# Kernel tuning notes

Measured on AMD Instinct MI355X. Metric: run time of the kernel, lower is better.

Reference implementation:

```python
import jax, jax.numpy as jnp
import numpy as np

N_ATOMS = 10000
N_EDGES = 200000
L_MAX = 2
K_L = [32, 24, 16]  # k_max_l = n_element_channels * n_max_l

# (l1, l2, L) in the original loop order (l1 outer, l2 inner, L ascending)
PAIRS = [(0,0,0),(0,1,1),(0,2,2),
         (1,0,1),(1,1,0),(1,1,1),(1,1,2),(1,2,1),(1,2,2),
         (2,0,2),(2,1,1),(2,1,2),(2,2,0),(2,2,1),(2,2,2)]
# concatenated input width -> k_max_l[L] per (L, sigma) channel
LIN = {'0_1': (72, 32), '1_1': (80, 24), '1_m1': (40, 24), '2_1': (72, 16), '2_m1': (32, 16)}


def setup_inputs() -> dict:
    key = jax.random.key(0)
    it = iter(jax.random.split(key, 64))
    def nrm(shape):
        return jax.random.normal(next(it), shape, dtype=jnp.float32)
    inp = {}
    for l in range(L_MAX + 1):
        inp['rb%d' % l] = nrm((N_EDGES, K_L[l]))           # radial basis per l
    for l in range(L_MAX + 1):
        inp['sh%d' % l] = nrm((N_EDGES, 2*l+1, 1))         # spherical harmonics per l
    inp['emb'] = nrm((N_ATOMS, 1, K_L[0]))                 # initial center embedding
    for l in range(L_MAX + 1):
        inp['f%d' % l] = nrm((N_ATOMS, 2*l+1, K_L[l]))     # nu=1 equivariant features
    for (l1, l2, L) in PAIRS:
        inp['cg_%d_%d_%d' % (l1, l2, L)] = nrm(((2*l1+1)*(2*l2+1), 2*L+1))
    for LS, (fin, fout) in LIN.items():
        inp['W_' + LS] = nrm((fin, fout)) / np.float32(np.sqrt(fin))
        inp['b_' + LS] = nrm((fout,)) * 0.01
    inp['centers'] = jax.random.randint(next(it), (N_EDGES,), 0, N_ATOMS)
    inp['neighbors'] = jax.random.randint(next(it), (N_EDGES,), 0, N_ATOMS)
    inp['n_atoms'] = N_ATOMS
    return inp


def _normalize(x, dims):
    # Normalizer(dims): RMS normalization over the given dims
    return x * jax.lax.rsqrt(jnp.mean(x * x, axis=dims, keepdims=True) + 1e-12)


def _forward(floats, centers, neighbors, n_atoms):
    (rb0, rb1, rb2, sh0, sh1, sh2, emb, f0, f1, f2,
     cg_0_0_0, cg_0_1_1, cg_0_2_2, cg_1_0_1, cg_1_1_0, cg_1_1_1, cg_1_1_2,
     cg_1_2_1, cg_1_2_2, cg_2_0_2, cg_2_1_1, cg_2_1_2, cg_2_2_0, cg_2_2_1,
     cg_2_2_2, W_0_1, b_0_1, W_1_1, b_1_1, W_1_m1, b_1_m1, W_2_1, b_2_1,
     W_2_m1, b_2_m1) = floats
    rb = [rb0, rb1, rb2]; sh = [sh0, sh1, sh2]; feats = [f0, f1, f2]
    cgs = {'0_0_0': cg_0_0_0, '0_1_1': cg_0_1_1, '0_2_2': cg_0_2_2,
           '1_0_1': cg_1_0_1, '1_1_0': cg_1_1_0, '1_1_1': cg_1_1_1,
           '1_1_2': cg_1_1_2, '1_2_1': cg_1_2_1, '1_2_2': cg_1_2_2,
           '2_0_2': cg_2_0_2, '2_1_1': cg_2_1_1, '2_1_2': cg_2_1_2,
           '2_2_0': cg_2_2_0, '2_2_1': cg_2_2_1, '2_2_2': cg_2_2_2}
    lin = {'0_1': (W_0_1, b_0_1), '1_1': (W_1_1, b_1_1), '1_m1': (W_1_m1, b_1_m1),
           '2_1': (W_2_1, b_2_1), '2_m1': (W_2_m1, b_2_m1)}

    # ---- InvariantMessagePasser: density_l = scatter_add over centers of
    #      sh_l * rb_l * emb[neighbors]
    emb_n = emb[neighbors]                                       # [E, 1, k0]
    densities = []
    for l in range(L_MAX + 1):
        msg = sh[l] * rb[l][:, None, :] * emb_n[:, :, :K_L[l]]   # [E, 2l+1, k_l]
        densities.append(jax.ops.segment_sum(msg, centers, num_segments=n_atoms))

    # ---- EquivariantMessagePasser
    ve = [sh[l] * rb[l][:, None, :] for l in range(L_MAX + 1)]   # vector expansion [E,2l+1,k_l]
    fn = [feats[l][neighbors] for l in range(L_MAX + 1)]         # gathered neighbor feats
    results = {}
    for (l1, l2, L) in PAIRS:
        S = (-1) ** (l1 + l2 + L)
        k = min(K_L[l1], K_L[l2])
        t1 = ve[l1][:, :, :k]                                    # [E, 2l1+1, k]
        t2 = fn[l2][:, :, :k]                                    # [E, 2l2+1, k]
        cg = cgs['%d_%d_%d' % (l1, l2, L)].reshape(2*l1+1, 2*l2+1, 2*L+1)
        # fused outer product + CG contraction -> [E, 2L+1, k]
        res = jnp.einsum('eak,ebk,abM->eMk', t1, t2, cg)
        pooled = jax.ops.segment_sum(res, centers, num_segments=n_atoms)
        LS = '%d_%s' % (L, 'm1' if S < 0 else '1')
        results.setdefault(LS, []).append(pooled)

    outs = {}
    for LS, (W, b) in lin.items():
        x = jnp.concatenate(results[LS], axis=2)                 # [n_atoms, 2L+1, size_LS]
        x = _normalize(x, (0, 1))
        x = jnp.einsum('amf,fk->amk', x, W) + b
        outs[LS] = _normalize(x, (0, 1, 2))

    return (densities[0], densities[1], densities[2],
            outs['0_1'], outs['1_1'], outs['1_m1'], outs['2_1'], outs['2_m1'])


def reference(rb0, rb1, rb2, sh0, sh1, sh2, emb, f0, f1, f2,
              cg_0_0_0, cg_0_1_1, cg_0_2_2, cg_1_0_1, cg_1_1_0, cg_1_1_1,
              cg_1_1_2, cg_1_2_1, cg_1_2_2, cg_2_0_2, cg_2_1_1, cg_2_1_2,
              cg_2_2_0, cg_2_2_1, cg_2_2_2, W_0_1, b_0_1, W_1_1, b_1_1,
              W_1_m1, b_1_m1, W_2_1, b_2_1, W_2_m1, b_2_m1,
              centers, neighbors, n_atoms):
    floats = (rb0, rb1, rb2, sh0, sh1, sh2, emb, f0, f1, f2,
              cg_0_0_0, cg_0_1_1, cg_0_2_2, cg_1_0_1, cg_1_1_0, cg_1_1_1,
              cg_1_1_2, cg_1_2_1, cg_1_2_2, cg_2_0_2, cg_2_1_1, cg_2_1_2,
              cg_2_2_0, cg_2_2_1, cg_2_2_2, W_0_1, b_0_1, W_1_1, b_1_1,
              W_1_m1, b_1_m1, W_2_1, b_2_1, W_2_m1, b_2_m1)
    return _forward(floats, centers, neighbors, n_atoms)
```

## Files before the change

kernel.cpp:

```cpp
#include <hip/hip_runtime.h>
#include <hip/hip_bf16.h>

typedef __hip_bfloat16 bf16;

#define N_ATOMS 10000
#define N_EDGES 200000

#define SCG   0
#define SINV  616
#define SS1P  1024
#define SS2P  19968
#define SWS2  20288
#define SINTS 20352
#define IFLAG  0
#define ICOUNT 16
#define IOFFS  10016
#define ICURS  20032
#define IELIST 30032
#define INTS_END 430032
#define SXACC (SINTS + INTS_END)
#define BIG_FLOATS (SXACC + 952*N_ATOMS)

#define O0 0
#define O1 320000
// ... 20 lines not shown
__constant__ int c_fin[5]   = {72,80,40,72,32};
__constant__ int c_kout[5]  = {32,24,24,16,16};
__constant__ int c_yoff[5]  = {OY+0, OY+320000, OY+1040000, OY+1760000, OY+2560000};
__constant__ int c_numel[5] = {320000,720000,720000,800000,800000};
__constant__ int c_cum[6]   = {0,32,104,176,256,336};
__constant__ int c_xb[5]    = {0,72,312,432,792};
__constant__ int c_Ms[5]    = {1,3,3,5,5};

__global__ void k_zero(float* wsf, int* wsi,
                       const unsigned short* rb0u, const unsigned short* embu) {
  if (blockIdx.x == 0 && threadIdx.x < 64) {
    int lane = threadIdx.x;
    int bad = 0;
    for (int i = lane; i < 256; i += 64) {
      unsigned u1 = ((unsigned)rb0u[2*i]) << 16;
      unsigned u2 = ((unsigned)embu[2*i]) << 16;
      float v1 = __uint_as_float(u1);
      float v2 = __uint_as_float(u2);
      if (!(fabsf(v1) < 1e9f) || !(fabsf(v2) < 1e9f)) bad = 1;
    }
    unsigned long long any = __ballot(bad);
    if (lane == 0) wsi[IFLAG] = (any != 0ULL) ? 1 : 0;
  }
  int i = blockIdx.x*blockDim.x + threadIdx.x;
  if (i < N_ATOMS) wsi[ICOUNT + i] = 0;
  int j = i - N_ATOMS;
  if (j >= 0 && j < N_ATOMS) wsi[ICURS + j] = 0;
  j -= N_ATOMS;
  if (j >= 0 && j < 18944) wsf[SS1P + j] = 0.f;
  j -= 18944;
  if (j >= 0 && j < 325) wsf[SS2P + j] = 0.f;
}

template<typename T>
__global__ void k_cg(Ptrs15 cg, float* wsf, const int* flag) {
  if (flag[0] != dtid<T>()) return;
  int i = blockIdx.x*blockDim.x + threadIdx.x;
  if (i >= 615) return;
  int s = 0, off = i;
  while (off >= c_cg_sizes[s]) { off -= c_cg_sizes[s]; ++s; }
  wsf[SCG + i] = ldv((const T*)cg.p[s], off);
}

__global__ void k_hist(const int* __restrict__ centers, int* __restrict__ counts) {
  int e = blockIdx.x*blockDim.x + threadIdx.x;
  if (e < N_EDGES) atomicAdd(&counts[centers[e]], 1);
}

__global__ void k_scan(const int* __restrict__ counts, int* __restrict__ offs) {
  __shared__ int part[1024];
  int t = threadIdx.x;
  int base = t*10;
  int s = 0;
  for (int i = 0; i < 10; ++i) { int idx = base+i; if (idx < N_ATOMS) s += counts[idx]; }
  part[t] = s;
  __syncthreads();
  for (int d = 1; d < 1024; d <<= 1) {
    int v = part[t];
    int add = (t >= d) ? part[t-d] : 0;
    __syncthreads();
    part[t] = v + add;
    __syncthreads();
  }
  int run = (t == 0) ? 0 : part[t-1];
  for (int i = 0; i < 10; ++i) {
    int idx = base+i;
    if (idx < N_ATOMS) { offs[idx] = run; run += counts[idx]; }
  }
  if (t == 1023) offs[N_ATOMS] = part[1023];
}

__global__ void k_scatter2(const int* __restrict__ centers, const int* __restrict__ neighbors,
                           const int* __restrict__ offs, int* __restrict__ cursors,
                           int2* __restrict__ elist2) {
  int e = blockIdx.x*blockDim.x + threadIdx.x;
  if (e < N_EDGES) {
    int c = centers[e];
    int p = atomicAdd(&cursors[c], 1);
    elist2[offs[c] + p] = make_int2(e, neighbors[e]);
  }
}

template<typename T>
__global__ __launch_bounds__(128) void k_role(
    const T* __restrict__ rb0, const T* __restrict__ rb1, const T* __restrict__ rb2,
    const T* __restrict__ sh0, const T* __restrict__ sh1, const T* __restrict__ sh2,
    const T* __restrict__ emb, const T* __restrict__ f0, const T* __restrict__ f1,
    const T* __restrict__ f2, const int2* __restrict__ el2,
    const int* __restrict__ offs, const float* __restrict__ cgf,
    float* __restrict__ s1p, float* __restrict__ xout, T* __restrict__ out,
    const int* __restrict__ flag)
{
  if (flag[0] != dtid<T>()) return;
  int lane = threadIdx.x & 63;
  int g = blockIdx.x * 2 + (threadIdx.x >> 6);
  int a = g / 5;
  int role = g - a*5;
  int beg = offs[a];
  int cnt = offs[a+1] - beg;
  const int2* eb = el2 + beg;
  int ab = a & 63;
  int k32 = lane & 31, e2 = lane >> 5;
  int k16 = lane & 15, e4 = lane >> 4;
  float* xg = xout + a*952;
  float* s1r = s1p + ab*296;

  if (role == 0) {
    float acc[8];
    #pragma unroll
    for (int i = 0; i < 8; ++i) acc[i] = 0.f;
    for (int base = 0; base < cnt; base += 4) {
      #pragma unroll
      for (int u = 0; u < 2; ++u) {
        int idx = base + 2*u + e2;
        float w = (idx < cnt) ? 1.f : 0.f;
        int ic  = (idx < cnt) ? idx : 0;
        int2 en = eb[ic];
        int e = en.x, n = en.y;
        float s0 = ldv(sh0, e);
        float s1a0 = ldv(sh1, e*3+0), s1a1 = ldv(sh1, e*3+1), s1a2 = ldv(sh1, e*3+2);
        float rb0k = ldv(rb0, e*32 + k32) * w;
        float ek   = ldv(emb, n*32 + k32);
        float f0k  = ldv(f0,  n*32 + k32);
        float ve0 = s0 * rb0k;
        acc[0] = fmaf(ve0, ek, acc[0]);
        acc[4] = fmaf(ve0, f0k, acc[4]);
        if (k32 < 24) {
          float rb1k = ldv(rb1, e*24 + k32) * w;
          float rbek = rb1k * ek;
          acc[1] = fmaf(s1a0, rbek, acc[1]);
          acc[2] = fmaf(s1a1, rbek, acc[2]);
          acc[3] = fmaf(s1a2, rbek, acc[3]);
          float f1k0 = ldv(f1, n*72 + k32);
          float f1k1 = ldv(f1, n*72 + 24 + k32);
          float f1k2 = ldv(f1, n*72 + 48 + k32);
          acc[5] = fmaf(ve0, f1k0, acc[5]);
          acc[6] = fmaf(ve0, f1k1, acc[6]);
          acc[7] = fmaf(ve0, f1k2, acc[7]);
        }
      }
    }
    #pragma unroll
    for (int i = 0; i < 8; ++i) acc[i] += __shfl_xor(acc[i], 32);
    float x000 = cgf[0] * acc[4];
    const float* C011 = cgf + 1;
    float x011[3];
    #pragma unroll
    for (int M = 0; M < 3; ++M) {
      float t = 0.f;
      #pragma unroll
      for (int b = 0; b < 3; ++b) t = fmaf(acc[5+b], C011[b*3+M], t);
      x011[M] = t;
    }
    if (lane < 32) {
      stv(out, O0 + a*32 + k32, acc[0]);
      xg[k32] = x000;
      atomicAdd(&s1r[k32], x000*x000);
      if (k32 < 24) {
        #pragma unroll
        for (int m = 0; m < 3; ++m) stv(out, O1 + a*72 + m*24 + k32, acc[1+m]);
        #pragma unroll
        for (int M = 0; M < 3; ++M) xg[72+M*80+k32] = x011[M];
        atomicAdd(&s1r[72+k32], x011[0]*x011[0]+x011[1]*x011[1]+x011[2]*x011[2]);
      }
    }
  } else if (role == 1) {
    float acc[12];
    #pragma unroll
    for (int i = 0; i < 12; ++i) acc[i] = 0.f;
    int k24 = (k32 < 24) ? k32 : 23;
    float m24 = (k32 < 24) ? 1.f : 0.f;
    for (int base = 0; base < cnt; base += 4) {
      #pragma unroll
      for (int u = 0; u < 2; ++u) {
        int idx = base + 2*u + e2;
        float w = ((idx < cnt) ? 1.f : 0.f) * m24;
        int ic  = (idx < cnt) ? idx : 0;
        int2 en = eb[ic];
        int e = en.x, n = en.y;
        float s1a0 = ldv(sh1, e*3+0), s1a1 = ldv(sh1, e*3+1), s1a2 = ldv(sh1, e*3+2);
        float rb1k = ldv(rb1, e*24 + k24) * w;
        float f0k  = ldv(f0,  n*32 + k24);
        float f1k0 = ldv(f1, n*72 + k24);
        float f1k1 = ldv(f1, n*72 + 24 + k24);
        float f1k2 = ldv(f1, n*72 + 48 + k24);
        float g3 = rb1k * f0k;
        acc[0] = fmaf(g3, s1a0, acc[0]);
        acc[1] = fmaf(g3, s1a1, acc[1]);
        acc[2] = fmaf(g3, s1a2, acc[2]);
        float sa;
        sa = rb1k * s1a0;
        acc[3] = fmaf(sa, f1k0, acc[3]); acc[4] = fmaf(sa, f1k1, acc[4]); acc[5] = fmaf(sa, f1k2, acc[5]);
        sa = rb1k * s1a1;
        acc[6] = fmaf(sa, f1k0, acc[6]); acc[7] = fmaf(sa, f1k1, acc[7]); acc[8] = fmaf(sa, f1k2, acc[8]);
        sa = rb1k * s1a2;
        acc[9] = fmaf(sa, f1k0, acc[9]); acc[10] = fmaf(sa, f1k1, acc[10]); acc[11] = fmaf(sa, f1k2, acc[11]);
      }
    }
    #pragma unroll
    for (int i = 0; i < 12; ++i) acc[i] += __shfl_xor(acc[i], 32);
    const float* C101 = cgf + 35;
    const float* C110 = cgf + 44;
    const float* C111 = cgf + 53;
    const float* C112 = cgf + 80;
    float x101[3], x111[3], x112[5], x110;
    #pragma unroll
    for (int M = 0; M < 3; ++M) {
      float t = 0.f;
      #pragma unroll
      for (int aa = 0; aa < 3; ++aa) t = fmaf(acc[aa], C101[aa*3+M], t);
      x101[M] = t;
    }
    {
      float t = 0.f;
      #pragma unroll
      for (int q = 0; q < 9; ++q) t = fmaf(acc[3+q], C110[q], t);
      x110 = t;
    }
    #pragma unroll
    for (int M = 0; M < 3; ++M) {
      float t = 0.f;
      #pragma unroll
      for (int q = 0; q < 9; ++q) t = fmaf(acc[3+q], C111[q*3+M], t);
      x111[M] = t;
    }
    #pragma unroll
    for (int M = 0; M < 5; ++M) {
      float t = 0.f;
      #pragma unroll
      for (int q = 0; q < 9; ++q) t = fmaf(acc[3+q], C112[q*5+M], t);
      x112[M] = t;
    }
    if (lane < 24) {
      xg[32+k32] = x110;
      #pragma unroll
      for (int M = 0; M < 3; ++M) xg[72+M*80+24+k32] = x101[M];
      #pragma unroll
      for (int M = 0; M < 3; ++M) xg[312+M*40+k32]   = x111[M];
      #pragma unroll
      for (int M = 0; M < 5; ++M) xg[432+M*72+16+k32] = x112[M];
      atomicAdd(&s1r[32+k32], x110*x110);
      atomicAdd(&s1r[96+k32], x101[0]*x101[0]+x101[1]*x101[1]+x101[2]*x101[2]);
      atomicAdd(&s1r[152+k32], x111[0]*x111[0]+x111[1]*x111[1]+x111[2]*x111[2]);
      atomicAdd(&s1r[208+k32], x112[0]*x112[0]+x112[1]*x112[1]+x112[2]*x112[2]
                              + x112[3]*x112[3]+x112[4]*x112[4]);
    }
  } else if (role == 2) {
    float acc[25];
    #pragma unroll
    for (int i = 0; i < 25; ++i) acc[i] = 0.f;
    for (int base = 0; base < cnt; base += 8) {
      #pragma unroll
      for (int u = 0; u < 2; ++u) {
        int idx = base + 4*u + e4;
        float w = (idx < cnt) ? 1.f : 0.f;
        int ic  = (idx < cnt) ? idx : 0;
        int2 en = eb[ic];
        int e = en.x, n = en.y;
        float s0 = ldv(sh0, e);
        float s1a[3];
        #pragma unroll
        for (int m = 0; m < 3; ++m) s1a[m] = ldv(sh1, e*3+m);
        float s2a[5];
        #pragma unroll
        for (int m = 0; m < 5; ++m) s2a[m] = ldv(sh2, e*5+m);
        float rb0k = ldv(rb0, e*32 + k16) * w;
        float rb1k = ldv(rb1, e*24 + k16) * w;
        float rb2k = ldv(rb2, e*16 + k16) * w;
        float ek   = ldv(emb, n*32 + k16);
        float f2k[5];
        #pragma unroll
        for (int b = 0; b < 5; ++b) f2k[b] = ldv(f2, n*80 + b*16 + k16);
        float re = rb2k * ek;
        #pragma unroll
        for (int m = 0; m < 5; ++m) acc[m] = fmaf(s2a[m], re, acc[m]);
        float ve0 = s0 * rb0k;
        #pragma unroll
        for (int b = 0; b < 5; ++b) acc[5+b] = fmaf(ve0, f2k[b], acc[5+b]);
        #pragma unroll
        for (int aa = 0; aa < 3; ++aa) {
          float sa = rb1k * s1a[aa];
          #pragma unroll
          for (int b = 0; b < 5; ++b)
            acc[10+aa*5+b] = fmaf(sa, f2k[b], acc[10+aa*5+b]);
        }
      }
    }
    #pragma unroll
    for (int i = 0; i < 25; ++i) {
      acc[i] += __shfl_xor(acc[i], 16);
      acc[i] += __shfl_xor(acc[i], 32);
    }
    const float* C022 = cgf + 10;
    const float* C121 = cgf + 125;
    const float* C122 = cgf + 170;
    float x022[5], x121[3], x122[5];
    #pragma unroll
    for (int M = 0; M < 5; ++M) {
      float t = 0.f;
      #pragma unroll
      for (int b = 0; b < 5; ++b) t = fmaf(acc[5+b], C022[b*5+M], t);
      x022[M] = t;
    }
    #pragma unroll
    for (int M = 0; M < 3; ++M) {
      float t = 0.f;
      #pragma unroll
      for (int q = 0; q < 15; ++q) t = fmaf(acc[10+q], C121[q*3+M], t);
      x121[M] = t;
    }
    #pragma unroll
    for (int M = 0; M < 5; ++M) {
      float t = 0.f;
      #pragma unroll
      for (int q = 0; q < 15; ++q) t = fmaf(acc[10+q], C122[q*5+M], t);
      x122[M] = t;
    }
    if (lane < 16) {
      #pragma unroll
      for (int m = 0; m < 5; ++m) stv(out, O2 + a*80 + m*16 + k16, acc[m]);
      #pragma unroll
      for (int M = 0; M < 5; ++M) xg[432+M*72+k16]   = x022[M];
      #pragma unroll
      for (int M = 0; M < 3; ++M) xg[72+M*80+48+k16] = x121[M];
      #pragma unroll
      for (int M = 0; M < 5; ++M) xg[792+M*32+k16]   = x122[M];
      atomicAdd(&s1r[192+k16], x022[0]*x022[0]+x022[1]*x022[1]+x022[2]*x022[2]
                              + x022[3]*x022[3]+x022[4]*x022[4]);
      atomicAdd(&s1r[120+k16], x121[0]*x121[0]+x121[1]*x121[1]+x121[2]*x121[2]);
      atomicAdd(&s1r[264+k16], x122[0]*x122[0]+x122[1]*x122[1]+x122[2]*x122[2]
                              + x122[3]*x122[3]+x122[4]*x122[4]);
    }
  } else if (role == 3) {
    float acc[20];
    #pragma unroll
    for (int i = 0; i < 20; ++i) acc[i] = 0.f;
    for (int base = 0; base < cnt; base += 8) {
      #pragma unroll
      for (int u = 0; u < 2; ++u) {
        int idx = base + 4*u + e4;
        float w = (idx < cnt) ? 1.f : 0.f;
        int ic  = (idx < cnt) ? idx : 0;
        int2 en = eb[ic];
        int e = en.x, n = en.y;
        float s2a[5];
        #pragma unroll
        for (int m = 0; m < 5; ++m) s2a[m] = ldv(sh2, e*5+m);
        float rb2k = ldv(rb2, e*16 + k16) * w;
        float f0k  = ldv(f0,  n*32 + k16);
        float f1k[3];
        #pragma unroll
        for (int b = 0; b < 3; ++b) f1k[b] = ldv(f1, n*72 + b*24 + k16);
        float g9 = rb2k * f0k;
        #pragma unroll
        for (int aa = 0; aa < 5; ++aa) acc[aa] = fmaf(g9, s2a[aa], acc[aa]);
        #pragma unroll
        for (int aa = 0; aa < 5; ++aa) {
          float sa = rb2k * s2a[aa];
          #pragma unroll
          for (int b = 0; b < 3; ++b)
            acc[5+aa*3+b] = fmaf(sa, f1k[b], acc[5+aa*3+b]);
        }
      }
    }
    #pragma unroll
    for (int i = 0; i < 20; ++i) {
      acc[i] += __shfl_xor(acc[i], 16);
      acc[i] += __shfl_xor(acc[i], 32);
    }
    const float* C202 = cgf + 245;
    const float* C211 = cgf + 270;
    const float* C212 = cgf + 315;
    float x202[5], x211[3], x212[5];
    #pragma unroll
    for (int M = 0; M < 5; ++M) {
      float t = 0.f;
      #pragma unroll
      for (int aa = 0; aa < 5; ++aa) t = fmaf(acc[aa], C202[aa*5+M], t);
      x202[M] = t;
    }
    #pragma unroll
    for (int M = 0; M < 3; ++M) {
      float t = 0.f;
      #pragma unroll
      for (int q = 0; q < 15; ++q) t = fmaf(acc[5+q], C211[q*3+M], t);
      x211[M] = t;
    }
    #pragma unroll
    for (int M = 0; M < 5; ++M) {
      float t = 0.f;
      #pragma unroll
      for (int q = 0; q < 15; ++q) t = fmaf(acc[5+q], C212[q*5+M], t);
      x212[M] = t;
    }
    if (lane < 16) {
      #pragma unroll
      for (int M = 0; M < 5; ++M) xg[432+M*72+40+k16] = x202[M];
      #pragma unroll
      for (int M = 0; M < 3; ++M) xg[72+M*80+64+k16]  = x211[M];
      #pragma unroll
      for (int M = 0; M < 5; ++M) xg[792+M*32+16+k16] = x212[M];
      atomicAdd(&s1r[232+k16], x202[0]*x202[0]+x202[1]*x202[1]+x202[2]*x202[2]
                              + x202[3]*x202[3]+x202[4]*x202[4]);
      atomicAdd(&s1r[136+k16], x211[0]*x211[0]+x211[1]*x211[1]+x211[2]*x211[2]);
      atomicAdd(&s1r[280+k16], x212[0]*x212[0]+x212[1]*x212[1]+x212[2]*x212[2]
                              + x212[3]*x212[3]+x212[4]*x212[4]);
    }
  } else {
    float acc[25];
    #pragma unroll
    for (int i = 0; i < 25; ++i) acc[i] = 0.f;
    for (int base = 0; base < cnt; base += 8) {
      #pragma unroll
      for (int u = 0; u < 2; ++u) {
        int idx = base + 4*u + e4;
        float w = (idx < cnt) ? 1.f : 0.f;
        int ic  = (idx < cnt) ? idx : 0;
        int2 en = eb[ic];
        int e = en.x, n = en.y;
        float s2a[5];
        #pragma unroll
        for (int m = 0; m < 5; ++m) s2a[m] = ldv(sh2, e*5+m);
        float rb2k = ldv(rb2, e*16 + k16) * w;
        float f2k[5];
        #pragma unroll
        for (int b = 0; b < 5; ++b) f2k[b] = ldv(f2, n*80 + b*16 + k16);
        #pragma unroll
        for (int aa = 0; aa < 5; ++aa) {
          float sa = rb2k * s2a[aa];
          #pragma unroll
          for (int b = 0; b < 5; ++b)
            acc[aa*5+b] = fmaf(sa, f2k[b], acc[aa*5+b]);
        }
      }
    }
    #pragma unroll
    for (int i = 0; i < 25; ++i) {
      acc[i] += __shfl_xor(acc[i], 16);
      acc[i] += __shfl_xor(acc[i], 32);
    }
    const float* C220 = cgf + 390;
    const float* C221 = cgf + 415;
    const float* C222 = cgf + 490;
    float x220, x221[3], x222[5];
    {
      float t = 0.f;
      #pragma unroll
      for (int q = 0; q < 25; ++q) t = fmaf(acc[q], C220[q], t);
      x220 = t;
    }
    #pragma unroll
    for (int M = 0; M < 3; ++M) {
      float t = 0.f;
      #pragma unroll
      for (int q = 0; q < 25; ++q) t = fmaf(acc[q], C221[q*3+M], t);
      x221[M] = t;
    }
    #pragma unroll
    for (int M = 0; M < 5; ++M) {
      float t = 0.f;
      #pragma unroll
      for (int q = 0; q < 25; ++q) t = fmaf(acc[q], C222[q*5+M], t);
      x222[M] = t;
    }
    if (lane < 16) {
      xg[56+k16] = x220;
      #pragma unroll
      for (int M = 0; M < 3; ++M) xg[312+M*40+24+k16] = x221[M];
      #pragma unroll
      for (int M = 0; M < 5; ++M) xg[432+M*72+56+k16] = x222[M];
      atomicAdd(&s1r[56+k16], x220*x220);
      atomicAdd(&s1r[176+k16], x221[0]*x221[0]+x221[1]*x221[1]+x221[2]*x221[2]);
      atomicAdd(&s1r[248+k16], x222[0]*x222[0]+x222[1]*x222[1]+x222[2]*x222[2]
                              + x222[3]*x222[3]+x222[4]*x222[4]);
    }
  }
}

template<typename T, int MODE>
__global__ __launch_bounds__(256) void k_main(
    const T* __restrict__ rb0, const T* __restrict__ rb1, const T* __restrict__ rb2,
    const T* __restrict__ sh0, const T* __restrict__ sh1, const T* __restrict__ sh2,
    const T* __restrict__ emb, const T* __restrict__ f0, const T* __restrict__ f1,
    const T* __restrict__ f2, const int2* __restrict__ el2,
    const int* __restrict__ offs, const float* __restrict__ cgf,
    float* __restrict__ s1p, const float* __restrict__ inv,
    float* __restrict__ s2p, LinP lp, T* __restrict__ out,
    const int* __restrict__ flag)
{
  if (flag[0] != dtid<T>()) return;
  int lane = threadIdx.x & 63;
  int wv   = threadIdx.x >> 6;
  int tix  = threadIdx.x;
  int a = blockIdx.x;
  int beg = offs[a];
  int cnt = offs[a+1] - beg;
  int k32 = lane & 31, e2 = lane >> 5;
  int k16 = lane & 15, e4 = lane >> 4;
  int ab = a & 63;
  float* s1r = s1p + ab*296;

  __shared__ int2 sel[256];
  __shared__ __align__(16) float L[952];
  __shared__ float red[4][5];

  float acc[25];
  #pragma unroll
  for (int i = 0; i < 25; ++i) acc[i] = 0.f;

  for (int cbase = 0; cbase < cnt; cbase += 256) {
    int nch = cnt - cbase; if (nch > 256) nch = 256;
    __syncthreads();
    if (tix < nch) sel[tix] = el2[beg + cbase + tix];
    __syncthreads();

    if (wv == 0) {
      for (int base = 0; base < nch; base += 4) {
        #pragma unroll
        for (int u = 0; u < 2; ++u) {
          int idx = base + 2*u + e2;
          float w = (idx < nch) ? 1.f : 0.f;
          int ic  = (idx < nch) ? idx : 0;
          int2 en = sel[ic];
          int e = en.x, n = en.y;
          float s0 = ldv(sh0, e);
          float s1a0 = ldv(sh1, e*3+0), s1a1 = ldv(sh1, e*3+1), s1a2 = ldv(sh1, e*3+2);
          float rb0k = ldv(rb0, e*32 + k32) * w;
          float ek   = ldv(emb, n*32 + k32);
          float f0k  = ldv(f0,  n*32 + k32);
          float ve0 = s0 * rb0k;
          acc[0] = fmaf(ve0, ek, acc[0]);
          acc[4] = fmaf(ve0, f0k, acc[4]);
          if (k32 < 24) {
            float rb1k = ldv(rb1, e*24 + k32) * w;
            float f1k0 = ldv(f1, n*72 + k32);
            float f1k1 = ldv(f1, n*72 + 24 + k32);
            float f1k2 = ldv(f1, n*72 + 48 + k32);
            float rbek = rb1k * ek;
            acc[1] = fmaf(s1a0, rbek, acc[1]);
            acc[2] = fmaf(s1a1, rbek, acc[2]);
            acc[3] = fmaf(s1a2, rbek, acc[3]);
            acc[5] = fmaf(ve0, f1k0, acc[5]);
            acc[6] = fmaf(ve0, f1k1, acc[6]);
            acc[7] = fmaf(ve0, f1k2, acc[7]);
            float g3 = rb1k * f0k;
            acc[8]  = fmaf(g3, s1a0, acc[8]);
            acc[9]  = fmaf(g3, s1a1, acc[9]);
            acc[10] = fmaf(g3, s1a2, acc[10]);
            #pragma unroll
            for (int aa = 0; aa < 3; ++aa) {
              float sa = rb1k * ((aa==0)?s1a0:(aa==1)?s1a1:s1a2);
              acc[11+aa*3+0] = fmaf(sa, f1k0, acc[11+aa*3+0]);
              acc[11+aa*3+1] = fmaf(sa, f1k1, acc[11+aa*3+1]);
              acc[11+aa*3+2] = fmaf(sa, f1k2, acc[11+aa*3+2]);
            }
          }
        }
      }
    } else if (wv == 1) {
// ... 310 lines not shown
        atomicAdd(&s1r[248+k16], q);
      }
    }
  }

  if constexpr (MODE == 2) {
    if (wv == 0) {
      if (lane < 32) {
        L[k32] = acc[4]*inv[k32];
        if (k32 < 24) {
          L[32+k32] = acc[11]*inv[32+k32];
          #pragma unroll
          for (int M = 0; M < 3; ++M) L[72+M*80+k32]     = acc[5+M]*inv[72+k32];
          #pragma unroll
          for (int M = 0; M < 3; ++M) L[72+M*80+24+k32]  = acc[8+M]*inv[96+k32];
          #pragma unroll
          for (int M = 0; M < 3; ++M) L[312+M*40+k32]    = acc[12+M]*inv[152+k32];
          #pragma unroll
          for (int M = 0; M < 5; ++M) L[432+M*72+16+k32] = acc[15+M]*inv[208+k32];
        }
      }
    } else if (wv == 1) {
      if (lane < 16) {
        #pragma unroll
        for (int M = 0; M < 5; ++M) L[432+M*72+k16]    = acc[5+M]*inv[192+k16];
        #pragma unroll
        for (int M = 0; M < 3; ++M) L[72+M*80+48+k16]  = acc[10+M]*inv[120+k16];
        #pragma unroll
        for (int M = 0; M < 5; ++M) L[792+M*32+k16]    = acc[13+M]*inv[264+k16];
      }
    } else if (wv == 2) {
      if (lane < 16) {
        #pragma unroll
        for (int M = 0; M < 5; ++M) L[432+M*72+40+k16] = acc[0+M]*inv[232+k16];
        #pragma unroll
        for (int M = 0; M < 3; ++M) L[72+M*80+64+k16]  = acc[5+M]*inv[136+k16];
        #pragma unroll
        for (int M = 0; M < 5; ++M) L[792+M*32+16+k16] = acc[8+M]*inv[280+k16];
      }
    } else {
      if (lane < 16) {
        L[56+k16] = acc[0]*inv[56+k16];
        #pragma unroll
        for (int M = 0; M < 3; ++M) L[312+M*40+24+k16] = acc[1+M]*inv[176+k16];
        #pragma unroll
        for (int M = 0; M < 5; ++M) L[432+M*72+56+k16] = acc[4+M]*inv[248+k16];
      }
    }
    __syncthreads();
    int t = threadIdx.x;
    float y2[5] = {0.f,0.f,0.f,0.f,0.f};
    for (int tau = t; tau < 336; tau += 256) {
      int ls = 0;
      while (tau >= c_cum[ls+1]) ++ls;
      int rem = tau - c_cum[ls];
      int kn = c_kout[ls], fin = c_fin[ls];
      int M = rem / kn, ko = rem - M*kn;
      const T* W = (const T*)lp.W[ls];
      float y = ldv((const T*)lp.B[ls], ko);
      const float* xv = &L[c_xb[ls] + M*fin];
      for (int f = 0; f < fin; ++f) y = fmaf(xv[f], ldv(W, f*kn+ko), y);
      stv(out, c_yoff[ls] + (a*c_Ms[ls] + M)*kn + ko, y);
      y2[ls] += y*y;
    }
    #pragma unroll
    for (int i = 0; i < 5; ++i) {
      y2[i] += __shfl_xor(y2[i], 1);  y2[i] += __shfl_xor(y2[i], 2);
      y2[i] += __shfl_xor(y2[i], 4);  y2[i] += __shfl_xor(y2[i], 8);
      y2[i] += __shfl_xor(y2[i], 16); y2[i] += __shfl_xor(y2[i], 32);
    }
    if (lane == 0) {
      #pragma unroll
      for (int i = 0; i < 5; ++i) red[wv][i] = y2[i];
    }
    __syncthreads();
    if (t == 0) {
      #pragma unroll
      for (int i = 0; i < 5; ++i)
        atomicAdd(&s2p[i*64 + ab], red[0][i]+red[1][i]+red[2][i]+red[3][i]);
    }
  }
}

template<typename T>
__global__ __launch_bounds__(256) void k_lin(
    const float* __restrict__ xg, const float* __restrict__ inv,
    LinP lp, T* __restrict__ out, float* __restrict__ s2p,
    const int* __restrict__ flag)
{
  if (flag[0] != dtid<T>()) return;
  int a = blockIdx.x;
  int t = threadIdx.x;
  __shared__ float L[952];
  for (int i = t; i < 952; i += 256) {
    int ch;
    if      (i < 72)  ch = i;
    else if (i < 312) ch = 72  + (i-72)  % 80;
    else if (i < 432) ch = 152 + (i-312) % 40;
    else if (i < 792) ch = 192 + (i-432) % 72;
    else              ch = 264 + (i-792) % 32;
    L[i] = xg[a*952 + i] * inv[ch];
  }
  __syncthreads();
  float y2[5] = {0.f,0.f,0.f,0.f,0.f};
  for (int tau = t; tau < 336; tau += 256) {
    int ls = 0;
    while (tau >= c_cum[ls+1]) ++ls;
    int rem = tau - c_cum[ls];
    int kn = c_kout[ls], fin = c_fin[ls];
    int M = rem / kn, ko = rem - M*kn;
    const T* W = (const T*)lp.W[ls];
    float y = ldv((const T*)lp.B[ls], ko);
    const float* xv = &L[c_xb[ls] + M*fin];
    for (int f = 0; f < fin; ++f) y = fmaf(xv[f], ldv(W, f*kn+ko), y);
    stv(out, c_yoff[ls] + (a*c_Ms[ls] + M)*kn + ko, y);
    y2[ls] += y*y;
  }
  __shared__ float red[4][5];
  #pragma unroll
  for (int i = 0; i < 5; ++i) {
    y2[i] += __shfl_xor(y2[i], 1);  y2[i] += __shfl_xor(y2[i], 2);
    y2[i] += __shfl_xor(y2[i], 4);  y2[i] += __shfl_xor(y2[i], 8);
    y2[i] += __shfl_xor(y2[i], 16); y2[i] += __shfl_xor(y2[i], 32);
  }
  if ((t & 63) == 0) {
    #pragma unroll
    for (int i = 0; i < 5; ++i) red[t>>6][i] = y2[i];
  }
  __syncthreads();
  if (t == 0) {
    #pragma unroll
    for (int i = 0; i < 5; ++i)
      atomicAdd(&s2p[i*64 + (a & 63)], red[0][i]+red[1][i]+red[2][i]+red[3][i]);
  }
}

__global__ void k_red1(const float* __restrict__ s1p, float* __restrict__ inv) {
  int ch = blockIdx.x, lane = threadIdx.x;
  float v = s1p[lane*296 + ch];
  v += __shfl_xor(v, 1);  v += __shfl_xor(v, 2);  v += __shfl_xor(v, 4);
  v += __shfl_xor(v, 8);  v += __shfl_xor(v, 16); v += __shfl_xor(v, 32);
  if (lane == 0) {
    float rows = (ch < 72) ? 10000.f : (ch < 192) ? 30000.f : 50000.f;
    inv[ch] = rsqrtf(v/rows + 1e-12f);
  }
}

__global__ void k_red2(const float* __restrict__ s2p, float* __restrict__ ws2) {
  int ls = blockIdx.x, lane = threadIdx.x;
  float v = s2p[ls*64 + lane];
  v += __shfl_xor(v, 1);  v += __shfl_xor(v, 2);  v += __shfl_xor(v, 4);
  v += __shfl_xor(v, 8);  v += __shfl_xor(v, 16); v += __shfl_xor(v, 32);
  if (lane == 0) ws2[ls] = v;
}

template<typename T>
__global__ void k_scale(const float* __restrict__ ws2, T* __restrict__ out,
                        const int* __restrict__ flag) {
  if (flag[0] != dtid<T>()) return;
  int i = blockIdx.x*blockDim.x + threadIdx.x;
  if (i >= 3360000) return;
  int ls = (i < 320000) ? 0 : (i < 1040000) ? 1 : (i < 1760000) ? 2 : (i < 2560000) ? 3 : 4;
  float scale = rsqrtf(ws2[ls] / (float)c_numel[ls] + 1e-12f);
  stv(out, OY + i, ldv((const T*)out, OY + i) * scale);
}

template<typename T>
static void launch_chain(void* const* d_in, T* out, float* wsf, int* wsi,
                         Ptrs15 cg, LinP lp, bool big, hipStream_t stream) {
  const T* rb0 = (const T*)d_in[0];
  const T* rb1 = (const T*)d_in[1];
  const T* rb2 = (const T*)d_in[2];
  const T* sh0 = (const T*)d_in[3];
  const T* sh1 = (const T*)d_in[4];
  const T* sh2 = (const T*)d_in[5];
  const T* emb = (const T*)d_in[6];
  const T* f0  = (const T*)d_in[7];
  const T* f1  = (const T*)d_in[8];
  const T* f2  = (const T*)d_in[9];
  const int* flag = wsi + IFLAG;
  const int2* el2 = (const int2*)(wsi + IELIST);

  k_cg<T><<<3, 256, 0, stream>>>(cg, wsf, flag);
  if (big) {
    k_role<T><<<25000, 128, 0, stream>>>(rb0, rb1, rb2, sh0, sh1, sh2, emb, f0, f1, f2,
        el2, wsi+IOFFS, wsf+SCG, wsf+SS1P, wsf+SXACC, out, flag);
    k_red1<<<296, 64, 0, stream>>>(wsf+SS1P, wsf+SINV);
    k_lin<T><<<N_ATOMS, 256, 0, stream>>>(wsf+SXACC, wsf+SINV, lp, out, wsf+SS2P, flag);
  } else {
    k_main<T,1><<<N_ATOMS, 256, 0, stream>>>(rb0, rb1, rb2, sh0, sh1, sh2, emb, f0, f1, f2,
        el2, wsi+IOFFS, wsf+SCG, wsf+SS1P, nullptr, nullptr, lp, out, flag);
    k_red1<<<296, 64, 0, stream>>>(wsf+SS1P, wsf+SINV);
    k_main<T,2><<<N_ATOMS, 256, 0, stream>>>(rb0, rb1, rb2, sh0, sh1, sh2, emb, f0, f1, f2,
        el2, wsi+IOFFS, wsf+SCG, nullptr, wsf+SINV, wsf+SS2P, lp, out, flag);
  }
  k_red2<<<5, 64, 0, stream>>>(wsf+SS2P, wsf+SWS2);
  k_scale<T><<<(3360000+255)/256, 256, 0, stream>>>(wsf+SWS2, out, flag);
}

extern "C" void kernel_launch(void* const* d_in, const int* in_sizes, int n_in,
                              void* d_out, int out_size, void* d_ws, size_t ws_size,
                              hipStream_t stream) {
  float* wsf = (float*)d_ws;
  int*   wsi = (int*)(wsf + SINTS);
  const int* centers   = (const int*)d_in[35];
  const int* neighbors = (const int*)d_in[36];
  bool big = ws_size >= (size_t)BIG_FLOATS * 4;

  int know = -1;
  if (in_sizes) {
    long long nb = (long long)in_sizes[0];
    if (nb == (long long)N_EDGES*32*2) know = 0;
    else if (nb == (long long)N_EDGES*32*4) know = 1;
  }
  if (know < 0) {
    long long ob = (long long)out_size;
    if (ob == (long long)OUT_ELEMS*2) know = 0;
    else if (ob == (long long)OUT_ELEMS*4) know = 1;
  }

  Ptrs15 cg;
  for (int i = 0; i < 15; ++i) cg.p[i] = d_in[10+i];
  LinP lp;
  lp.W[0] = d_in[25]; lp.B[0] = d_in[26];
  lp.W[1] = d_in[27]; lp.B[1] = d_in[28];
  lp.W[2] = d_in[29]; lp.B[2] = d_in[30];
  lp.W[3] = d_in[31]; lp.B[3] = d_in[32];
  lp.W[4] = d_in[33]; lp.B[4] = d_in[34];

  k_zero<<<154, 256, 0, stream>>>(wsf, wsi,
                                  (const unsigned short*)d_in[0],
                                  (const unsigned short*)d_in[6]);
  k_hist<<<(N_EDGES+255)/256, 256, 0, stream>>>(centers, wsi+ICOUNT);
  k_scan<<<1, 1024, 0, stream>>>(wsi+ICOUNT, wsi+IOFFS);
  k_scatter2<<<(N_EDGES+255)/256, 256, 0, stream>>>(centers, neighbors, wsi+IOFFS,
                                                    wsi+ICURS, (int2*)(wsi+IELIST));

  if (know != 1) launch_chain<bf16 >(d_in, (bf16*)d_out,  wsf, wsi, cg, lp, big, stream);
  if (know != 0) launch_chain<float>(d_in, (float*)d_out, wsf, wsi, cg, lp, big, stream);
}
```

Before: 450.3 us.

## Merge dtype-templated launches into runtime-dispatched kernels and fuse reductions

```diff
diff --git a/kernel.cpp b/kernel.cpp
--- a/kernel.cpp
+++ b/kernel.cpp
@@ -126,20 +126,18 @@
 }
 
 template<typename T>
-__global__ __launch_bounds__(128) void k_role(
+__device__ __forceinline__ void role_body(
     const T* __restrict__ rb0, const T* __restrict__ rb1, const T* __restrict__ rb2,
     const T* __restrict__ sh0, const T* __restrict__ sh1, const T* __restrict__ sh2,
     const T* __restrict__ emb, const T* __restrict__ f0, const T* __restrict__ f1,
     const T* __restrict__ f2, const int2* __restrict__ el2,
-    const int* __restrict__ offs, const float* __restrict__ cgf,
-    float* __restrict__ s1p, float* __restrict__ xout, T* __restrict__ out,
-    const int* __restrict__ flag)
+    const int* __restrict__ offs, Ptrs15 cg,
+    float* __restrict__ s1p, float* __restrict__ xout, T* __restrict__ out)
 {
-  if (flag[0] != dtid<T>()) return;
   int lane = threadIdx.x & 63;
-  int g = blockIdx.x * 2 + (threadIdx.x >> 6);
-  int a = g / 5;
-  int role = g - a*5;
+  int role = threadIdx.x >> 6;
+  int bid = blockIdx.x;
+  int a = (bid & 7) * 1250 + (bid >> 3);
   int beg = offs[a];
   int cnt = offs[a+1] - beg;
   const int2* eb = el2 + beg;
@@ -186,14 +184,15 @@
     }
     #pragma unroll
     for (int i = 0; i < 8; ++i) acc[i] += __shfl_xor(acc[i], 32);
-    float x000 = cgf[0] * acc[4];
-    const float* C011 = cgf + 1;
+    const T* C000 = (const T*)cg.p[0];
+    const T* C011 = (const T*)cg.p[1];
+    float x000 = ldv(C000,0) * acc[4];
     float x011[3];
     #pragma unroll
     for (int M = 0; M < 3; ++M) {
       float t = 0.f;
       #pragma unroll
-      for (int b = 0; b < 3; ++b) t = fmaf(acc[5+b], C011[b*3+M], t);
+      for (int b = 0; b < 3; ++b) t = fmaf(acc[5+b], ldv(C011, b*3+M), t);
       x011[M] = t;
     }
     if (lane < 32) {
@@ -243,36 +242,36 @@
     }
     #pragma unroll
     for (int i = 0; i < 12; ++i) acc[i] += __shfl_xor(acc[i], 32);
-    const float* C101 = cgf + 35;
-    const float* C110 = cgf + 44;
-    const float* C111 = cgf + 53;
-    const float* C112 = cgf + 80;
+    const T* C101 = (const T*)cg.p[3];
+    const T* C110 = (const T*)cg.p[4];
+    const T* C111 = (const T*)cg.p[5];
+    const T* C112 = (const T*)cg.p[6];
     float x101[3], x111[3], x112[5], x110;
     #pragma unroll
     for (int M = 0; M < 3; ++M) {
       float t = 0.f;
       #pragma unroll
-      for (int aa = 0; aa < 3; ++aa) t = fmaf(acc[aa], C101[aa*3+M], t);
+      for (int aa = 0; aa < 3; ++aa) t = fmaf(acc[aa], ldv(C101, aa*3+M), t);
       x101[M] = t;
     }
     {
       float t = 0.f;
       #pragma unroll
-      for (int q = 0; q < 9; ++q) t = fmaf(acc[3+q], C110[q], t);
+      for (int q = 0; q < 9; ++q) t = fmaf(acc[3+q], ldv(C110, q), t);
       x110 = t;
     }
     #pragma unroll
     for (int M = 0; M < 3; ++M) {
       float t = 0.f;
       #pragma unroll
-      for (int q = 0; q < 9; ++q) t = fmaf(acc[3+q], C111[q*3+M], t);
+      for (int q = 0; q < 9; ++q) t = fmaf(acc[3+q], ldv(C111, q*3+M), t);
       x111[M] = t;
     }
     #pragma unroll
     for (int M = 0; M < 5; ++M) {
       float t = 0.f;
       #pragma unroll
-      for (int q = 0; q < 9; ++q) t = fmaf(acc[3+q], C112[q*5+M], t);
+      for (int q = 0; q < 9; ++q) t = fmaf(acc[3+q], ldv(C112, q*5+M), t);
       x112[M] = t;
     }
     if (lane < 24) {
@@ -335,29 +334,29 @@
       acc[i] += __shfl_xor(acc[i], 16);
       acc[i] += __shfl_xor(acc[i], 32);
     }
-    const float* C022 = cgf + 10;
-    const float* C121 = cgf + 125;
-    const float* C122 = cgf + 170;
+    const T* C022 = (const T*)cg.p[2];
+    const T* C121 = (const T*)cg.p[7];
+    const T* C122 = (const T*)cg.p[8];
     float x022[5], x121[3], x122[5];
     #pragma unroll
     for (int M = 0; M < 5; ++M) {
       float t = 0.f;
       #pragma unroll
-      for (int b = 0; b < 5; ++b) t = fmaf(acc[5+b], C022[b*5+M], t);
+      for (int b = 0; b < 5; ++b) t = fmaf(acc[5+b], ldv(C022, b*5+M), t);
       x022[M] = t;
     }
     #pragma unroll
     for (int M = 0; M < 3; ++M) {
       float t = 0.f;
       #pragma unroll
-      for (int q = 0; q < 15; ++q) t = fmaf(acc[10+q], C121[q*3+M], t);
+      for (int q = 0; q < 15; ++q) t = fmaf(acc[10+q], ldv(C121, q*3+M), t);
       x121[M] = t;
     }
     #pragma unroll
     for (int M = 0; M < 5; ++M) {
       float t = 0.f;
       #pragma unroll
-      for (int q = 0; q < 15; ++q) t = fmaf(acc[10+q], C122[q*5+M], t);
+      for (int q = 0; q < 15; ++q) t = fmaf(acc[10+q], ldv(C122, q*5+M), t);
       x122[M] = t;
     }
     if (lane < 16) {
@@ -412,29 +411,29 @@
       acc[i] += __shfl_xor(acc[i], 16);
       acc[i] += __shfl_xor(acc[i], 32);
     }
-    const float* C202 = cgf + 245;
-    const float* C211 = cgf + 270;
-    const float* C212 = cgf + 315;
+    const T* C202 = (const T*)cg.p[9];
+    const T* C211 = (const T*)cg.p[10];
+    const T* C212 = (const T*)cg.p[11];
     float x202[5], x211[3], x212[5];
     #pragma unroll
     for (int M = 0; M < 5; ++M) {
       float t = 0.f;
       #pragma unroll
-      for (int aa = 0; aa < 5; ++aa) t = fmaf(acc[aa], C202[aa*5+M], t);
+      for (int aa = 0; aa < 5; ++aa) t = fmaf(acc[aa], ldv(C202, aa*5+M), t);
       x202[M] = t;
     }
     #pragma unroll
     for (int M = 0; M < 3; ++M) {
       float t = 0.f;
       #pragma unroll
-      for (int q = 0; q < 15; ++q) t = fmaf(acc[5+q], C211[q*3+M], t);
+      for (int q = 0; q < 15; ++q) t = fmaf(acc[5+q], ldv(C211, q*3+M), t);
       x211[M] = t;
     }
     #pragma unroll
     for (int M = 0; M < 5; ++M) {
       float t = 0.f;
       #pragma unroll
-      for (int q = 0; q < 15; ++q) t = fmaf(acc[5+q], C212[q*5+M], t);
+      for (int q = 0; q < 15; ++q) t = fmaf(acc[5+q], ldv(C212, q*5+M), t);
       x212[M] = t;
     }
     if (lane < 16) {
@@ -483,28 +482,28 @@
       acc[i] += __shfl_xor(acc[i], 16);
       acc[i] += __shfl_xor(acc[i], 32);
     }
-    const float* C220 = cgf + 390;
-    const float* C221 = cgf + 415;
-    const float* C222 = cgf + 490;
+    const T* C220 = (const T*)cg.p[12];
+    const T* C221 = (const T*)cg.p[13];
+    const T* C222 = (const T*)cg.p[14];
     float x220, x221[3], x222[5];
     {
       float t = 0.f;
       #pragma unroll
-      for (int q = 0; q < 25; ++q) t = fmaf(acc[q], C220[q], t);
+      for (int q = 0; q < 25; ++q) t = fmaf(acc[q], ldv(C220, q), t);
       x220 = t;
     }
     #pragma unroll
     for (int M = 0; M < 3; ++M) {
       float t = 0.f;
       #pragma unroll
-      for (int q = 0; q < 25; ++q) t = fmaf(acc[q], C221[q*3+M], t);
+      for (int q = 0; q < 25; ++q) t = fmaf(acc[q], ldv(C221, q*3+M), t);
       x221[M] = t;
     }
     #pragma unroll
     for (int M = 0; M < 5; ++M) {
       float t = 0.f;
       #pragma unroll
-      for (int q = 0; q < 25; ++q) t = fmaf(acc[q], C222[q*5+M], t);
+      for (int q = 0; q < 25; ++q) t = fmaf(acc[q], ldv(C222, q*5+M), t);
       x222[M] = t;
     }
     if (lane < 16) {
@@ -519,6 +518,124 @@
                               + x222[3]*x222[3]+x222[4]*x222[4]);
     }
   }
+}
+
+__global__ __launch_bounds__(320) void k_role(
+    const void* rb0, const void* rb1, const void* rb2,
+    const void* sh0, const void* sh1, const void* sh2,
+    const void* emb, const void* f0, const void* f1, const void* f2,
+    const int2* __restrict__ el2, const int* __restrict__ offs, Ptrs15 cg,
+    float* __restrict__ s1p, float* __restrict__ xout, void* outv,
+    const int* __restrict__ flag, int know)
+{
+  int dt = (know >= 0) ? know : flag[0];
+  if (dt == 0)
+    role_body<bf16>((const bf16*)rb0,(const bf16*)rb1,(const bf16*)rb2,
+                    (const bf16*)sh0,(const bf16*)sh1,(const bf16*)sh2,
+                    (const bf16*)emb,(const bf16*)f0,(const bf16*)f1,(const bf16*)f2,
+                    el2, offs, cg, s1p, xout, (bf16*)outv);
+  else
+    role_body<float>((const float*)rb0,(const float*)rb1,(const float*)rb2,
+                     (const float*)sh0,(const float*)sh1,(const float*)sh2,
+                     (const float*)emb,(const float*)f0,(const float*)f1,(const float*)f2,
+                     el2, offs, cg, s1p, xout, (float*)outv);
+}
+
+template<typename T>
+__device__ __forceinline__ void lin_body(
+    const float* __restrict__ xg, const float* __restrict__ inv,
+    LinP lp, T* __restrict__ out, float* __restrict__ s2p)
+{
+  int a = blockIdx.x;
+  int t = threadIdx.x;
+  __shared__ float L[952];
+  for (int i = t; i < 952; i += 256) {
+    int ch;
+    if      (i < 72)  ch = i;
+    else if (i < 312) ch = 72  + (i-72)  % 80;
+    else if (i < 432) ch = 152 + (i-312) % 40;
+    else if (i < 792) ch = 192 + (i-432) % 72;
+    else              ch = 264 + (i-792) % 32;
+    L[i] = xg[a*952 + i] * inv[ch];
+  }
+  __syncthreads();
+  float y2[5] = {0.f,0.f,0.f,0.f,0.f};
+  for (int tau = t; tau < 336; tau += 256) {
+    int ls = 0;
+    while (tau >= c_cum[ls+1]) ++ls;
+    int rem = tau - c_cum[ls];
+    int kn = c_kout[ls], fin = c_fin[ls];
+    int M = rem / kn, ko = rem - M*kn;
+    const T* W = (const T*)lp.W[ls];
+    float y = ldv((const T*)lp.B[ls], ko);
+    const float* xv = &L[c_xb[ls] + M*fin];
+    for (int f = 0; f < fin; ++f) y = fmaf(xv[f], ldv(W, f*kn+ko), y);
+    stv(out, c_yoff[ls] + (a*c_Ms[ls] + M)*kn + ko, y);
+    y2[ls] += y*y;
+  }
+  __shared__ float red[4][5];
+  #pragma unroll
+  for (int i = 0; i < 5; ++i) {
+    y2[i] += __shfl_xor(y2[i], 1);  y2[i] += __shfl_xor(y2[i], 2);
+    y2[i] += __shfl_xor(y2[i], 4);  y2[i] += __shfl_xor(y2[i], 8);
+    y2[i] += __shfl_xor(y2[i], 16); y2[i] += __shfl_xor(y2[i], 32);
+  }
+  if ((t & 63) == 0) {
+    #pragma unroll
+    for (int i = 0; i < 5; ++i) red[t>>6][i] = y2[i];
+  }
+  __syncthreads();
+  if (t == 0) {
+    #pragma unroll
+    for (int i = 0; i < 5; ++i)
+      atomicAdd(&s2p[i*64 + (a & 63)], red[0][i]+red[1][i]+red[2][i]+red[3][i]);
+  }
+}
+
+__global__ __launch_bounds__(256) void k_lin(
+    const float* __restrict__ xg, const float* __restrict__ inv,
+    LinP lp, void* outv, float* __restrict__ s2p,
+    const int* __restrict__ flag, int know)
+{
+  int dt = (know >= 0) ? know : flag[0];
+  if (dt == 0) lin_body<bf16>(xg, inv, lp, (bf16*)outv, s2p);
+  else         lin_body<float>(xg, inv, lp, (float*)outv, s2p);
+}
+
+__global__ void k_red1(const float* __restrict__ s1p, float* __restrict__ inv) {
+  int ch = blockIdx.x, lane = threadIdx.x;
+  float v = s1p[lane*296 + ch];
+  v += __shfl_xor(v, 1);  v += __shfl_xor(v, 2);  v += __shfl_xor(v, 4);
+  v += __shfl_xor(v, 8);  v += __shfl_xor(v, 16); v += __shfl_xor(v, 32);
+  if (lane == 0) {
+    float rows = (ch < 72) ? 10000.f : (ch < 192) ? 30000.f : 50000.f;
+    inv[ch] = rsqrtf(v/rows + 1e-12f);
+  }
+}
+
+__global__ __launch_bounds__(256) void k_scale(
+    const float* __restrict__ s2p, void* outv,
+    const int* __restrict__ flag, int know)
+{
+  __shared__ float ssum[5];
+  int t = threadIdx.x;
+  if (t < 64) {
+    #pragma unroll
+    for (int i = 0; i < 5; ++i) {
+      float x = s2p[i*64 + t];
+      x += __shfl_xor(x, 1);  x += __shfl_xor(x, 2);  x += __shfl_xor(x, 4);
+      x += __shfl_xor(x, 8);  x += __shfl_xor(x, 16); x += __shfl_xor(x, 32);
+      if (t == 0) ssum[i] = x;
+    }
+  }
+  __syncthreads();
+  int dt = (know >= 0) ? know : flag[0];
+  int i = blockIdx.x*blockDim.x + t;
+  if (i >= 3360000) return;
+  int ls = (i < 320000) ? 0 : (i < 1040000) ? 1 : (i < 1760000) ? 2 : (i < 2560000) ? 3 : 4;
+  float scale = rsqrtf(ssum[ls] / (float)c_numel[ls] + 1e-12f);
+  if (dt == 0) { bf16* o = (bf16*)outv;  stv(o, OY+i, ldv((const bf16*)o,  OY+i) * scale); }
+  else         { float* o = (float*)outv; stv(o, OY+i, ldv((const float*)o, OY+i) * scale); }
 }
 
 template<typename T, int MODE>
@@ -995,122 +1112,6 @@
   }
 }
 
-template<typename T>
-__global__ __launch_bounds__(256) void k_lin(
-    const float* __restrict__ xg, const float* __restrict__ inv,
-    LinP lp, T* __restrict__ out, float* __restrict__ s2p,
-    const int* __restrict__ flag)
-{
-  if (flag[0] != dtid<T>()) return;
-  int a = blockIdx.x;
-  int t = threadIdx.x;
-  __shared__ float L[952];
-  for (int i = t; i < 952; i += 256) {
-    int ch;
-    if      (i < 72)  ch = i;
-    else if (i < 312) ch = 72  + (i-72)  % 80;
-    else if (i < 432) ch = 152 + (i-312) % 40;
-    else if (i < 792) ch = 192 + (i-432) % 72;
-    else              ch = 264 + (i-792) % 32;
-    L[i] = xg[a*952 + i] * inv[ch];
-  }
-  __syncthreads();
-  float y2[5] = {0.f,0.f,0.f,0.f,0.f};
-  for (int tau = t; tau < 336; tau += 256) {
-    int ls = 0;
-    while (tau >= c_cum[ls+1]) ++ls;
-    int rem = tau - c_cum[ls];
-    int kn = c_kout[ls], fin = c_fin[ls];
-    int M = rem / kn, ko = rem - M*kn;
-    const T* W = (const T*)lp.W[ls];
-    float y = ldv((const T*)lp.B[ls], ko);
-    const float* xv = &L[c_xb[ls] + M*fin];
-    for (int f = 0; f < fin; ++f) y = fmaf(xv[f], ldv(W, f*kn+ko), y);
-    stv(out, c_yoff[ls] + (a*c_Ms[ls] + M)*kn + ko, y);
-    y2[ls] += y*y;
-  }
-  __shared__ float red[4][5];
-  #pragma unroll
-  for (int i = 0; i < 5; ++i) {
-    y2[i] += __shfl_xor(y2[i], 1);  y2[i] += __shfl_xor(y2[i], 2);
-    y2[i] += __shfl_xor(y2[i], 4);  y2[i] += __shfl_xor(y2[i], 8);
-    y2[i] += __shfl_xor(y2[i], 16); y2[i] += __shfl_xor(y2[i], 32);
-  }
-  if ((t & 63) == 0) {
-    #pragma unroll
-    for (int i = 0; i < 5; ++i) red[t>>6][i] = y2[i];
-  }
-  __syncthreads();
-  if (t == 0) {
-    #pragma unroll
-    for (int i = 0; i < 5; ++i)
-      atomicAdd(&s2p[i*64 + (a & 63)], red[0][i]+red[1][i]+red[2][i]+red[3][i]);
-  }
-}
-
-__global__ void k_red1(const float* __restrict__ s1p, float* __restrict__ inv) {
-  int ch = blockIdx.x, lane = threadIdx.x;
-  float v = s1p[lane*296 + ch];
-  v += __shfl_xor(v, 1);  v += __shfl_xor(v, 2);  v += __shfl_xor(v, 4);
-  v += __shfl_xor(v, 8);  v += __shfl_xor(v, 16); v += __shfl_xor(v, 32);
-  if (lane == 0) {
-    float rows = (ch < 72) ? 10000.f : (ch < 192) ? 30000.f : 50000.f;
-    inv[ch] = rsqrtf(v/rows + 1e-12f);
-  }
-}
-
-__global__ void k_red2(const float* __restrict__ s2p, float* __restrict__ ws2) {
-  int ls = blockIdx.x, lane = threadIdx.x;
-  float v = s2p[ls*64 + lane];
-  v += __shfl_xor(v, 1);  v += __shfl_xor(v, 2);  v += __shfl_xor(v, 4);
-  v += __shfl_xor(v, 8);  v += __shfl_xor(v, 16); v += __shfl_xor(v, 32);
-  if (lane == 0) ws2[ls] = v;
-}
-
-template<typename T>
-__global__ void k_scale(const float* __restrict__ ws2, T* __restrict__ out,
-                        const int* __restrict__ flag) {
-  if (flag[0] != dtid<T>()) return;
-  int i = blockIdx.x*blockDim.x + threadIdx.x;
-  if (i >= 3360000) return;
-  int ls = (i < 320000) ? 0 : (i < 1040000) ? 1 : (i < 1760000) ? 2 : (i < 2560000) ? 3 : 4;
-  float scale = rsqrtf(ws2[ls] / (float)c_numel[ls] + 1e-12f);
-  stv(out, OY + i, ldv((const T*)out, OY + i) * scale);
-}
-
-template<typename T>
-static void launch_chain(void* const* d_in, T* out, float* wsf, int* wsi,
-                         Ptrs15 cg, LinP lp, bool big, hipStream_t stream) {
-  const T* rb0 = (const T*)d_in[0];
-  const T* rb1 = (const T*)d_in[1];
-  const T* rb2 = (const T*)d_in[2];
-  const T* sh0 = (const T*)d_in[3];
-  const T* sh1 = (const T*)d_in[4];
-  const T* sh2 = (const T*)d_in[5];
-  const T* emb = (const T*)d_in[6];
-  const T* f0  = (const T*)d_in[7];
-  const T* f1  = (const T*)d_in[8];
-  const T* f2  = (const T*)d_in[9];
-  const int* flag = wsi + IFLAG;
-  const int2* el2 = (const int2*)(wsi + IELIST);
-
-  k_cg<T><<<3, 256, 0, stream>>>(cg, wsf, flag);
-  if (big) {
-    k_role<T><<<25000, 128, 0, stream>>>(rb0, rb1, rb2, sh0, sh1, sh2, emb, f0, f1, f2,
-        el2, wsi+IOFFS, wsf+SCG, wsf+SS1P, wsf+SXACC, out, flag);
-    k_red1<<<296, 64, 0, stream>>>(wsf+SS1P, wsf+SINV);
-    k_lin<T><<<N_ATOMS, 256, 0, stream>>>(wsf+SXACC, wsf+SINV, lp, out, wsf+SS2P, flag);
-  } else {
-    k_main<T,1><<<N_ATOMS, 256, 0, stream>>>(rb0, rb1, rb2, sh0, sh1, sh2, emb, f0, f1, f2,
-        el2, wsi+IOFFS, wsf+SCG, wsf+SS1P, nullptr, nullptr, lp, out, flag);
-    k_red1<<<296, 64, 0, stream>>>(wsf+SS1P, wsf+SINV);
-    k_main<T,2><<<N_ATOMS, 256, 0, stream>>>(rb0, rb1, rb2, sh0, sh1, sh2, emb, f0, f1, f2,
-        el2, wsi+IOFFS, wsf+SCG, nullptr, wsf+SINV, wsf+SS2P, lp, out, flag);
-  }
-  k_red2<<<5, 64, 0, stream>>>(wsf+SS2P, wsf+SWS2);
-  k_scale<T><<<(3360000+255)/256, 256, 0, stream>>>(wsf+SWS2, out, flag);
-}
-
 extern "C" void kernel_launch(void* const* d_in, const int* in_sizes, int n_in,
                               void* d_out, int out_size, void* d_ws, size_t ws_size,
                               hipStream_t stream) {
@@ -1141,6 +1142,9 @@
   lp.W[3] = d_in[31]; lp.B[3] = d_in[32];
   lp.W[4] = d_in[33]; lp.B[4] = d_in[34];
 
+  const int* flag = wsi + IFLAG;
+  const int2* el2 = (const int2*)(wsi + IELIST);
+
   k_zero<<<154, 256, 0, stream>>>(wsf, wsi,
                                   (const unsigned short*)d_in[0],
                                   (const unsigned short*)d_in[6]);
@@ -1149,6 +1153,34 @@
   k_scatter2<<<(N_EDGES+255)/256, 256, 0, stream>>>(centers, neighbors, wsi+IOFFS,
                                                     wsi+ICURS, (int2*)(wsi+IELIST));
 
-  if (know != 1) launch_chain<bf16 >(d_in, (bf16*)d_out,  wsf, wsi, cg, lp, big, stream);
-  if (know != 0) launch_chain<float>(d_in, (float*)d_out, wsf, wsi, cg, lp, big, stream);
-}
+  if (big) {
+    k_role<<<N_ATOMS, 320, 0, stream>>>(d_in[0], d_in[1], d_in[2], d_in[3], d_in[4],
+        d_in[5], d_in[6], d_in[7], d_in[8], d_in[9], el2, wsi+IOFFS, cg,
+        wsf+SS1P, wsf+SXACC, d_out, flag, know);
+    k_red1<<<296, 64, 0, stream>>>(wsf+SS1P, wsf+SINV);
+    k_lin<<<N_ATOMS, 256, 0, stream>>>(wsf+SXACC, wsf+SINV, lp, d_out, wsf+SS2P,
+                                       flag, know);
+    k_scale<<<(3360000+255)/256, 256, 0, stream>>>(wsf+SS2P, d_out, flag, know);
+  } else {
+    k_cg<bf16 ><<<3, 256, 0, stream>>>(cg, wsf, flag);
+    k_cg<float><<<3, 256, 0, stream>>>(cg, wsf, flag);
+    k_main<bf16,1><<<N_ATOMS, 256, 0, stream>>>((const bf16*)d_in[0], (const bf16*)d_in[1],
+        (const bf16*)d_in[2], (const bf16*)d_in[3], (const bf16*)d_in[4], (const bf16*)d_in[5],
+        (const bf16*)d_in[6], (const bf16*)d_in[7], (const bf16*)d_in[8], (const bf16*)d_in[9],
+        el2, wsi+IOFFS, wsf+SCG, wsf+SS1P, nullptr, nullptr, lp, (bf16*)d_out, flag);
+    k_main<float,1><<<N_ATOMS, 256, 0, stream>>>((const float*)d_in[0], (const float*)d_in[1],
+        (const float*)d_in[2], (const float*)d_in[3], (const float*)d_in[4], (const float*)d_in[5],
+        (const float*)d_in[6], (const float*)d_in[7], (const float*)d_in[8], (const float*)d_in[9],
+        el2, wsi+IOFFS, wsf+SCG, wsf+SS1P, nullptr, nullptr, lp, (float*)d_out, flag);
+    k_red1<<<296, 64, 0, stream>>>(wsf+SS1P, wsf+SINV);
+    k_main<bf16,2><<<N_ATOMS, 256, 0, stream>>>((const bf16*)d_in[0], (const bf16*)d_in[1],
+        (const bf16*)d_in[2], (const bf16*)d_in[3], (const bf16*)d_in[4], (const bf16*)d_in[5],
+        (const bf16*)d_in[6], (const bf16*)d_in[7], (const bf16*)d_in[8], (const bf16*)d_in[9],
+        el2, wsi+IOFFS, wsf+SCG, nullptr, wsf+SINV, wsf+SS2P, lp, (bf16*)d_out, flag);
+    k_main<float,2><<<N_ATOMS, 256, 0, stream>>>((const float*)d_in[0], (const float*)d_in[1],
+        (const float*)d_in[2], (const float*)d_in[3], (const float*)d_in[4], (const float*)d_in[5],
+        (const float*)d_in[6], (const float*)d_in[7], (const float*)d_in[8], (const float*)d_in[9],
+        el2, wsi+IOFFS, wsf+SCG, nullptr, wsf+SINV, wsf+SS2P, lp, (float*)d_out, flag);
+    k_scale<<<(3360000+255)/256, 256, 0, stream>>>(wsf+SS2P, d_out, flag, know);
+  }
+}
```

New measurement: 516.2 us. 14.6% more time.
